# Kernel tuning notes

Hardware: AMD Instinct MI355X
Metric: run time of the kernel (lower is better)

The kernel has to match this reference:

```python
import jax, jax.numpy as jnp
import numpy as np

HOP = 768
NCB = 14
DIM = 512
VOCAB = 1024
W_SCALE = 0.02  # keep conv stacks numerically tame


def conv1d(x, w, b, stride=1, padding=0):
    # x: [B,C,L], w: [O,I,K] (torch layout), b: [O]
    y = jax.lax.conv_general_dilated(
        x, w, window_strides=(stride,), padding=[(padding, padding)],
        dimension_numbers=('NCH', 'OIH', 'NCH'))
    return y + b[None, :, None]


def conv_transpose1d(x, w, b, stride, padding):
    # torch ConvTranspose1d weight layout: (in, out, k)
    k = w.shape[2]
    w2 = jnp.flip(jnp.transpose(w, (1, 0, 2)), axis=2)  # -> OIH
    y = jax.lax.conv_general_dilated(
        x, w2, window_strides=(1,),
        padding=[(k - 1 - padding, k - 1 - padding)],
        lhs_dilation=(stride,),
        dimension_numbers=('NCH', 'OIH', 'NCH'))
    return y + b[None, :, None]


def setup_inputs() -> dict:
    key = jax.random.key(0)
    ks = jax.random.split(key, 16)
    f = lambda k, shp, s=W_SCALE: jax.random.normal(k, shp, dtype=jnp.float32) * s
    B, T = 2, 98304  # T = 768 * 128
    return {
        'audio': jax.random.normal(ks[0], (B, 1, T), dtype=jnp.float32),
        'codebooks': jax.random.normal(ks[1], (NCB, VOCAB, DIM), dtype=jnp.float32),
        'ew1': f(ks[2], (256, 1, 7)), 'eb1': f(ks[3], (256,)),
        'ew2': f(ks[4], (512, 256, 5)), 'eb2': f(ks[5], (512,)),
        'ew3': f(ks[6], (NCB * DIM, 512, 3)), 'eb3': f(ks[7], (NCB * DIM,)),
        'dw1': f(ks[8], (NCB * DIM, 512, 5)), 'db1': f(ks[9], (512,)),
        'dw2': f(ks[10], (256, 512, 5)), 'db2': f(ks[11], (256,)),
        'dw3': f(ks[12], (1, 256, 7)), 'db3': f(ks[13], (1,)),
    }


def reference(audio, codebooks, ew1, eb1, ew2, eb2, ew3, eb3,
              dw1, db1, dw2, db2, dw3, db3):
    B = audio.shape[0]
    # ---- encoder ----
    h = jax.nn.relu(conv1d(audio, ew1, eb1, stride=1, padding=3))
    h = jax.nn.relu(conv1d(h, ew2, eb2, stride=HOP, padding=2))
    h = conv1d(h, ew3, eb3, stride=1, padding=1)          # [B, NCB*DIM, S]
    S = h.shape[-1]
    emb = h.reshape(B, NCB, DIM, S).transpose(0, 1, 3, 2)  # [B, NCB, S, DIM]
    # ---- VQ: per-codebook squared L2 distance + argmin (same argmin as cdist) ----
    d2 = (jnp.sum(emb * emb, axis=-1, keepdims=True)            # [B,NCB,S,1]
          - 2.0 * jnp.einsum('bksd,kvd->bksv', emb, codebooks)  # [B,NCB,S,V]
          + jnp.sum(codebooks * codebooks, axis=-1)[None, :, None, :])
    codes = jnp.argmin(d2, axis=-1)                        # [B, NCB, S] int
    # ---- decode: embedding lookup + transposed conv decoder ----
    q = codebooks[jnp.arange(NCB)[None, :, None], codes]   # [B, NCB, S, DIM]
    q = q.transpose(0, 1, 3, 2).reshape(B, NCB * DIM, S)   # [B, NCB*DIM, S]
    a = jax.nn.relu(conv_transpose1d(q, dw1, db1, stride=HOP, padding=2))
    a = jax.nn.relu(conv1d(a, dw2, db2, stride=1, padding=2))
    a = jnp.tanh(conv1d(a, dw3, db3, stride=1, padding=3))
    return a  # [B, 1, (S-1)*HOP + 1]
```

## Files before the change

### kernel.cpp

```cpp
#include <hip/hip_runtime.h>
#include <hip/hip_bf16.h>
#include <math.h>

#define T_IN 98304
#define SS 128
#define NBATCH 2
#define NN 256
#define C1 256
#define C2 512
#define C3 7168
#define NCBK 14
#define DIMV 512
#define VOC 1024
#define TOUT 97537
#define HOP 768

#define OFF_CBN    0L
#define OFF_AB1    14336L
#define OFF_AB2    14848L
#define OFF_CCONST 15104L
#define OFF_H2C    15120L
#define OFF_H2XH   146192L
#define OFF_H2XL   342800L
#define OFF_H3H    539408L
#define OFF_H3L    1456912L
#define OFF_SCORES 2374416L
#define OFF_X1H    2374416L
#define OFF_X1L    2538256L
#define OFF_EW3PH  2374416L
#define OFF_EW3PL  5126928L
#define OFF_DW1T   539408L
#define OFF_XH     539408L
#define OFF_XL     3488528L
#define OFF_CODES  9714448L
#define OFF_QBF    9718032L
#define OFF_A1RAW  10635536L
#define OFF_A2ACT  11290896L

typedef __attribute__((ext_vector_type(8))) short short8;
typedef __attribute__((ext_vector_type(4))) float f32x4;

static __device__ inline ushort f2bf(float x) {
  __hip_bfloat16 h = __float2bfloat16(x);
  return *reinterpret_cast<ushort*>(&h);
}

static __device__ inline void split8(const float4 x0, const float4 x1,
                                     short8& h, short8& l) {
  float xs[8] = {x0.x, x0.y, x0.z, x0.w, x1.x, x1.y, x1.z, x1.w};
  #pragma unroll
  for (int e = 0; e < 8; ++e) {
    uint b = __float_as_uint(xs[e]);
    h[e] = (short)(b >> 16);
    float r = xs[e] - __uint_as_float(b & 0xffff0000u);
    l[e] = (short)(__float_as_uint(r) >> 16);
  }
}

__global__ void k_cbn(const float* __restrict__ cb, float* __restrict__ cbn) {
  int row = blockIdx.x * 4 + (threadIdx.x >> 6);
  int lane = threadIdx.x & 63;
  const float* p = cb + (long)row * DIMV;
  float s = 0.f;
  for (int d = lane; d < DIMV; d += 64) { float x = p[d]; s += x * x; }
  for (int off = 32; off; off >>= 1) s += __shfl_down(s, off);
  if (lane == 0) cbn[row] = s;
}

__global__ __launch_bounds__(256) void k_prep_ab2(const float* __restrict__ db1,
    const float* __restrict__ dw2, const float* __restrict__ db2,
    float* __restrict__ ab1, float* __restrict__ ab2) {
  __shared__ float red[256];
  int o = blockIdx.x, t = threadIdx.x;
  if (o == 0) { ab1[t] = fmaxf(db1[t], 0.f); ab1[t + 256] = fmaxf(db1[t + 256], 0.f); }
  const float* wp = dw2 + (long)o * C2 * 5;
  float acc = 0.f;
  #pragma unroll
  for (int h = 0; h < 2; ++h) {
    int c = t + h * 256;
    const float* p = wp + c * 5;
    float wsum = p[0] + p[1] + p[2] + p[3] + p[4];
    acc = fmaf(wsum, fmaxf(db1[c], 0.f), acc);
  }
  red[t] = acc;
  __syncthreads();
  for (int off = 128; off; off >>= 1) {
    if (t < off) red[t] += red[t + off];
    __syncthreads();
  }
  if (t == 0) ab2[o] = fmaxf(red[0] + db2[o], 0.f);
}

__global__ __launch_bounds__(256) void k_prep_c(const float* __restrict__ dw3,
    const float* __restrict__ db3, const float* __restrict__ ab2,
    float* __restrict__ cconst) {
  __shared__ float red[256];
  int t = threadIdx.x;
  float wsum3 = 0.f;
  #pragma unroll
  for (int j = 0; j < 7; ++j) wsum3 += dw3[t*7+j];
  red[t] = wsum3 * ab2[t];
  __syncthreads();
  for (int off = 128; off; off >>= 1) {
    if (t < off) red[t] += red[t + off];
    __syncthreads();
  }
  if (t == 0) cconst[0] = tanhf(red[0] + db3[0]);
}

__global__ __launch_bounds__(256) void k_enc1(const float* __restrict__ audio,
    const float* __restrict__ ew1, const float* __restrict__ eb1,
    ushort* __restrict__ X1h, ushort* __restrict__ X1l) {
  int n = blockIdx.x, ic = threadIdx.x;
  int b = n >> 7, s = n & 127;
  const float* ap = audio + (long)b * T_IN;
  int base = HOP * s - 5;
  float a[11];
  #pragma unroll
  for (int w = 0; w < 11; ++w) {
    int ai = base + w;
    a[w] = (ai >= 0 && ai < T_IN) ? ap[ai] : 0.f;
  }
  float w1[7];
  #pragma unroll
  for (int j = 0; j < 7; ++j) w1[j] = ew1[ic*7+j];
  float b1 = eb1[ic];
  long off = (long)n * 1280 + ic * 5;
  #pragma unroll
  for (int jj = 0; jj < 5; ++jj) {
    int tcol = HOP * s + jj - 2;
    float v = 0.f;
    if (tcol >= 0) {
      float acc = b1;
      #pragma unroll
      for (int j = 0; j < 7; ++j) acc = fmaf(w1[j], a[jj + j], acc);
      v = fmaxf(acc, 0.f);
    }
    uint bi = __float_as_uint(v);
    X1h[off + jj] = (ushort)(bi >> 16);
    float r = v - __uint_as_float(bi & 0xffff0000u);
    X1l[off + jj] = (ushort)(__float_as_uint(r) >> 16);
  }
}

__global__ __launch_bounds__(256) void gemm_enc2(const float* __restrict__ ew2,
    const ushort* __restrict__ X1h, const ushort* __restrict__ X1l,
    const float* __restrict__ eb2, float* __restrict__ h2c) {
  __shared__ __align__(16) float red[4 * 2048];
  const int tid = threadIdx.x;
  const int w = tid >> 6, lane = tid & 63;
  const int l15 = lane & 15, quad = lane >> 4;
  const int m0 = blockIdx.x * 32, n0 = blockIdx.y * 64;
  const int kbase = w * 320;
  f32x4 acc[2][4] = {};
  const float*  aB = ew2 + (long)(m0 + l15) * 1280 + kbase + quad * 8;
  const ushort* bhB = X1h + (long)(n0 + l15) * 1280 + kbase + quad * 8;
  const ushort* blB = X1l + (long)(n0 + l15) * 1280 + kbase + quad * 8;
  for (int k0 = 0; k0 < 320; k0 += 32) {
    short8 ah[2], al[2], bh[4], bl[4];
    #pragma unroll
    for (int f = 0; f < 2; ++f) {
      const float* ap = aB + (long)f * 16 * 1280 + k0;
      float4 x0 = *(const float4*)ap;
      float4 x1 = *(const float4*)(ap + 4);
      split8(x0, x1, ah[f], al[f]);
    }
    #pragma unroll
    for (int f = 0; f < 4; ++f) {
      bh[f] = *(const short8*)(bhB + (long)f * 16 * 1280 + k0);
      bl[f] = *(const short8*)(blB + (long)f * 16 * 1280 + k0);
    }
    #pragma unroll
    for (int i = 0; i < 2; ++i)
      #pragma unroll
      for (int j = 0; j < 4; ++j) {
        acc[i][j] = __builtin_amdgcn_mfma_f32_16x16x32_bf16(ah[i], bh[j], acc[i][j], 0, 0, 0);
        acc[i][j] = __builtin_amdgcn_mfma_f32_16x16x32_bf16(ah[i], bl[j], acc[i][j], 0, 0, 0);
        acc[i][j] = __builtin_amdgcn_mfma_f32_16x16x32_bf16(al[i], bh[j], acc[i][j], 0, 0, 0);
      }
  }
  #pragma unroll
  for (int i = 0; i < 2; ++i)
    #pragma unroll
    for (int j = 0; j < 4; ++j)
      *(float4*)&red[w * 2048 + (i * 4 + j) * 256 + lane * 4] = *(float4*)&acc[i][j];
  __syncthreads();
  #pragma unroll
  for (int q = 0; q < 2; ++q) {
    const int c = 2 * w + q;
    const int i = c >> 2, j = c & 3;
    float4 s = make_float4(0.f, 0.f, 0.f, 0.f);
    #pragma unroll
    for (int g = 0; g < 4; ++g) {
      float4 t4 = *(const float4*)&red[g * 2048 + c * 256 + lane * 4];
      s.x += t4.x; s.y += t4.y; s.z += t4.z; s.w += t4.w;
    }
    const int obase = m0 + i * 16 + quad * 4;
    float4 bias = *(const float4*)(eb2 + obase);
    const int n = n0 + j * 16 + l15;
    float4 out;
    out.x = fmaxf(s.x + bias.x, 0.f);
    out.y = fmaxf(s.y + bias.y, 0.f);
    out.z = fmaxf(s.z + bias.z, 0.f);
    out.w = fmaxf(s.w + bias.w, 0.f);
    *(float4*)(h2c + (long)n * C2 + obase) = out;
  }
}

__global__ void k_h2x(const float* __restrict__ h2c, ushort* __restrict__ h2xph,
                      ushort* __restrict__ h2xpl) {
  int idx = blockIdx.x * 256 + threadIdx.x;
  const int total = NN * 1536;
  for (; idx < total; idx += gridDim.x * 256) {
    int grp = idx >> 9;
    int r = idx & 511;
    int e = r & 7, lane = r >> 3;
    int quad = lane >> 4, l15 = lane & 15;
    int nt = grp / 48, kt = grp - nt * 48;
    int n = nt * 16 + l15;
    int k = kt * 32 + quad * 8 + e;
    int ic = k / 3, j = k - ic * 3;
    int s2 = (n & 127) + j - 1;
    int b = n >> 7;
    float v = (s2 >= 0 && s2 < SS) ? h2c[(long)(b*SS + s2)*C2 + ic] : 0.f;
    uint bi = __float_as_uint(v);
    h2xph[idx] = (ushort)(bi >> 16);
    float rr = v - __uint_as_float(bi & 0xffff0000u);
    h2xpl[idx] = (ushort)(__float_as_uint(rr) >> 16);
  }
}

__global__ __launch_bounds__(256) void k_ew3p(const float* __restrict__ ew3,
    ushort* __restrict__ ph, ushort* __restrict__ pl, int mrow0) {
  int o8 = blockIdx.x * 256 + threadIdx.x;
  const int total = 3584 * 1536 / 8;
  if (o8 >= total) return;
  int frag = o8 >> 6, lane = o8 & 63;
  int quad = lane >> 4, l15 = lane & 15;
  int mtL = frag / 48, kt = frag - mtL * 48;
  int m = mrow0 + mtL * 16 + l15;
  int k = kt * 32 + quad * 8;
  const float* s = ew3 + (long)m * 1536 + k;
  float4 x0 = *(const float4*)s;
  float4 x1 = *(const float4*)(s + 4);
  short8 h, l;
  split8(x0, x1, h, l);
  long off = (long)o8 * 8;
  *(short8*)(ph + off) = h;
  *(short8*)(pl + off) = l;
}

__global__ __launch_bounds__(256) void gemm_h3(const ushort* __restrict__ aH,
    const ushort* __restrict__ aL, const ushort* __restrict__ bH,
    const ushort* __restrict__ bL, const float* __restrict__ eb3,
    ushort* __restrict__ h3ph, ushort* __restrict__ h3pl, int mrow0) {
  __shared__ __align__(16) float red[4 * 4096];
  const int tid = threadIdx.x;
  const int w = tid >> 6, lane = tid & 63;
  const int l15 = lane & 15, quad = lane >> 4;
  const int bid = blockIdx.x;
  const int xcd = bid & 7, q = bid >> 3;
  const int mchunk = xcd * 7 + (q >> 2);
  const int nchunk = q & 3;
  const int mtL0 = mchunk * 4, nt0 = nchunk * 4, n0 = nchunk * 64;
  const int kt0 = w * 12;
  f32x4 acc[4][4] = {};
  const ushort* aHB = aH + ((long)(mtL0 * 48 + kt0)) * 512 + lane * 8;
  const ushort* aLB = aL + ((long)(mtL0 * 48 + kt0)) * 512 + lane * 8;
  const ushort* bHB = bH + ((long)(nt0 * 48 + kt0)) * 512 + lane * 8;
  const ushort* bLB = bL + ((long)(nt0 * 48 + kt0)) * 512 + lane * 8;
  for (int kt = 0; kt < 12; ++kt) {
    short8 ah[4], al[4], bh[4], bl[4];
    #pragma unroll
    for (int f = 0; f < 4; ++f) {
      long o = ((long)(f * 48 + kt)) * 512;
      ah[f] = *(const short8*)(aHB + o);
      al[f] = *(const short8*)(aLB + o);
      bh[f] = *(const short8*)(bHB + o);
      bl[f] = *(const short8*)(bLB + o);
    }
    #pragma unroll
    for (int i = 0; i < 4; ++i)
      #pragma unroll
      for (int j = 0; j < 4; ++j) {
        acc[i][j] = __builtin_amdgcn_mfma_f32_16x16x32_bf16(ah[i], bh[j], acc[i][j], 0, 0, 0);
        acc[i][j] = __builtin_amdgcn_mfma_f32_16x16x32_bf16(ah[i], bl[j], acc[i][j], 0, 0, 0);
        acc[i][j] = __builtin_amdgcn_mfma_f32_16x16x32_bf16(al[i], bh[j], acc[i][j], 0, 0, 0);
      }
  }
  #pragma unroll
  for (int i = 0; i < 4; ++i)
    #pragma unroll
    for (int j = 0; j < 4; ++j)
      *(float4*)&red[w * 4096 + (i * 4 + j) * 256 + lane * 4] = *(float4*)&acc[i][j];
  __syncthreads();
  const int mg0 = mrow0 + mchunk * 64 + w * 16 + quad * 4;
  float4 bias = *(const float4*)(eb3 + mg0);
  const int ktS = mg0 >> 5, quadk = (mg0 >> 3) & 3, es = mg0 & 7;
  #pragma unroll
  for (int j = 0; j < 4; ++j) {
    float4 s = *(const float4*)&red[(w * 4 + j) * 256 + lane * 4];
    #pragma unroll
    for (int r = 1; r < 4; ++r) {
      float4 tt = *(const float4*)&red[r * 4096 + (w * 4 + j) * 256 + lane * 4];
      s.x += tt.x; s.y += tt.y; s.z += tt.z; s.w += tt.w;
    }
    const int n = n0 + j * 16 + l15;
    float v0 = s.x + bias.x;
    float v1 = s.y + bias.y;
    float v2 = s.z + bias.z;
    float v3 = s.w + bias.w;
    uint b0 = __float_as_uint(v0), b1 = __float_as_uint(v1);
    uint b2 = __float_as_uint(v2), b3 = __float_as_uint(v3);
    uint2 hp;
    hp.x = (b0 >> 16) | (b1 & 0xffff0000u);
    hp.y = (b2 >> 16) | (b3 & 0xffff0000u);
    float r0 = v0 - __uint_as_float(b0 & 0xffff0000u);
    float r1 = v1 - __uint_as_float(b1 & 0xffff0000u);
    float r2 = v2 - __uint_as_float(b2 & 0xffff0000u);
    float r3 = v3 - __uint_as_float(b3 & 0xffff0000u);
    uint2 lp;
    lp.x = (__float_as_uint(r0) >> 16) | (__float_as_uint(r1) & 0xffff0000u);
    lp.y = (__float_as_uint(r2) >> 16) | (__float_as_uint(r3) & 0xffff0000u);
    long off = ((long)((n >> 4) * 224 + ktS)) * 512 + (quadk * 16 + (n & 15)) * 8 + es;
    *(uint2*)(h3ph + off) = hp;
    *(uint2*)(h3pl + off) = lp;
  }
}

__global__ __launch_bounds__(256) void gemm_scores(const float* __restrict__ cb,
    const ushort* __restrict__ h3ph, const ushort* __restrict__ h3pl,
    const float* __restrict__ cbn, float* __restrict__ scores) {
  __shared__ __align__(16) float red[4 * 4096];
  const int tid = threadIdx.x;
  const int w = tid >> 6, lane = tid & 63;
  const int l15 = lane & 15, quad = lane >> 4;
  const int m0 = blockIdx.x * 64, n0 = blockIdx.y * 64, z = blockIdx.z;
  const int kbase = w * 128;
  f32x4 acc[4][4] = {};
  const float*  aB = cb + (long)z * VOC * DIMV + (long)(m0 + l15) * 512 + kbase + quad * 8;
  const ushort* bHB = h3ph + ((long)((n0 >> 4) * 224 + z * 16 + (kbase >> 5))) * 512 + lane * 8;
  const ushort* bLB = h3pl + ((long)((n0 >> 4) * 224 + z * 16 + (kbase >> 5))) * 512 + lane * 8;
  for (int k0 = 0; k0 < 128; k0 += 32) {
    short8 ah[4], al[4], bh[4], bl[4];
    #pragma unroll
    for (int f = 0; f < 4; ++f) {
      const float* ap = aB + (long)f * 16 * 512 + k0;
      float4 x0 = *(const float4*)ap;
      float4 x1 = *(const float4*)(ap + 4);
      split8(x0, x1, ah[f], al[f]);
      long o = ((long)(f * 224) + (k0 >> 5)) * 512;
      bh[f] = *(const short8*)(bHB + o);
      bl[f] = *(const short8*)(bLB + o);
    }
    #pragma unroll
    for (int i = 0; i < 4; ++i)
      #pragma unroll
      for (int j = 0; j < 4; ++j) {
        acc[i][j] = __builtin_amdgcn_mfma_f32_16x16x32_bf16(ah[i], bh[j], acc[i][j], 0, 0, 0);
        acc[i][j] = __builtin_amdgcn_mfma_f32_16x16x32_bf16(ah[i], bl[j], acc[i][j], 0, 0, 0);
        acc[i][j] = __builtin_amdgcn_mfma_f32_16x16x32_bf16(al[i], bh[j], acc[i][j], 0, 0, 0);
      }
  }
  #pragma unroll
  for (int i = 0; i < 4; ++i)
    #pragma unroll
    for (int j = 0; j < 4; ++j)
      *(float4*)&red[w * 4096 + (i * 4 + j) * 256 + lane * 4] = *(float4*)&acc[i][j];
  __syncthreads();
  const int vbase = m0 + w * 16 + quad * 4;
  float4 cn = *(const float4*)(cbn + z * VOC + vbase);
  #pragma unroll
  for (int j = 0; j < 4; ++j) {
    float4 s = *(const float4*)&red[(w * 4 + j) * 256 + lane * 4];
    #pragma unroll
    for (int r = 1; r < 4; ++r) {
      float4 tt = *(const float4*)&red[r * 4096 + (w * 4 + j) * 256 + lane * 4];
      s.x += tt.x; s.y += tt.y; s.z += tt.z; s.w += tt.w;
    }
    const int n = n0 + j * 16 + l15;
    float4 out;
    out.x = cn.x - 2.f * s.x;
    out.y = cn.y - 2.f * s.y;
    out.z = cn.z - 2.f * s.z;
    out.w = cn.w - 2.f * s.w;
    *(float4*)(scores + ((long)z * NN + n) * VOC + vbase) = out;
  }
}

__global__ void k_argmin(const float* __restrict__ scores, int* __restrict__ codes) {
  int row = blockIdx.x;
  int lane = threadIdx.x;
  const float* p = scores + (long)row * VOC;
  float best = 3.4e38f; int bi = 0;
  for (int i = 0; i < 16; ++i) {
    int v = i * 64 + lane;
    float x = p[v];
    if (x < best) { best = x; bi = v; }
  }
  for (int off = 32; off; off >>= 1) {
    float ob = __shfl_down(best, off);
    int oi = __shfl_down(bi, off);
    if (ob < best || (ob == best && oi < bi)) { best = ob; bi = oi; }
  }
  if (lane == 0) codes[row] = bi;
}

__global__ __launch_bounds__(256) void k_dw1t(const float* __restrict__ dw1,
                                              ushort* __restrict__ dw1p) {
  __shared__ __align__(16) ushort T[64 * 72];
  int t = threadIdx.x;
  int k0 = blockIdx.x * 64, m0 = blockIdx.y * 64;
  int kk = t >> 2, mj = (t & 3) * 16;
  const float* src = dw1 + (long)(k0 + kk) * 2560 + m0 + mj;
  float x[16];
  *(float4*)&x[0]  = *(const float4*)(src);
  *(float4*)&x[4]  = *(const float4*)(src + 4);
  *(float4*)&x[8]  = *(const float4*)(src + 8);
  *(float4*)&x[12] = *(const float4*)(src + 12);
  #pragma unroll
  for (int l = 0; l < 16; ++l)
    T[(mj + l) * 72 + kk] = f2bf(x[l]);
  __syncthreads();
  int mo = t >> 2, kc = (t & 3) * 16;
  const int m = m0 + mo;
  const int mt = m >> 4, l15 = m & 15;
  #pragma unroll
  for (int h = 0; h < 2; ++h) {
    const int kk0 = kc + h * 8;
    const int kglob = k0 + kk0;
    const int kt = kglob >> 5;
    const int quad = (kglob >> 3) & 3;
    uint4 u = *(const uint4*)&T[mo * 72 + kk0];
    *(uint4*)(dw1p + ((long)(mt * 224 + kt)) * 512 + (quad * 16 + l15) * 8) = u;
  }
}

__global__ void k_gather_qbf(const float* __restrict__ cb, const int* __restrict__ codes,
                             ushort* __restrict__ qp) {
  int o = blockIdx.x * 256 + threadIdx.x;
  const int total = NN * C3 / 8;
  if (o >= total) return;
  int frag = o >> 6, r = o & 63;
  int quad = r >> 4, l15 = r & 15;
  int nt = frag / 224, kt = frag - nt * 224;
  int n = nt * 16 + l15;
  int kglob = kt * 32 + quad * 8;
  int kcb = kglob >> 9, d0 = kglob & 511;
  int code = codes[kcb * NN + n];
  const float* s = cb + ((long)(kcb * VOC + code)) * DIMV + d0;
  float4 x0 = *(const float4*)s;
  float4 x1 = *(const float4*)(s + 4);
  uint4 u;
  u.x = (uint)f2bf(x0.x) | ((uint)f2bf(x0.y) << 16);
  u.y = (uint)f2bf(x0.z) | ((uint)f2bf(x0.w) << 16);
  u.z = (uint)f2bf(x1.x) | ((uint)f2bf(x1.y) << 16);
  u.w = (uint)f2bf(x1.z) | ((uint)f2bf(x1.w) << 16);
  ((uint4*)qp)[o] = u;
}

__global__ __launch_bounds__(1024) void gemm_a1_mfma(const ushort* __restrict__ dw1p,
    const ushort* __restrict__ qp, float* __restrict__ a1raw) {
  __shared__ __align__(16) float red[4 * 4096];
  const int tid = threadIdx.x;
  const int w = tid >> 6, lane = tid & 63;
  const int l15 = lane & 15, quad = lane >> 4;
  const int mt0 = blockIdx.x * 4, nt0 = blockIdx.y * 4;
  const int kt0 = w * 14;
  f32x4 acc[4][4] = {};
  const ushort* aB = dw1p + ((long)(mt0 * 224 + kt0)) * 512 + lane * 8;
  const ushort* bB = qp   + ((long)(nt0 * 224 + kt0)) * 512 + lane * 8;
  #pragma unroll 2
  for (int kt = 0; kt < 14; ++kt) {
    short8 ah[4], bh[4];
    #pragma unroll
    for (int f = 0; f < 4; ++f) {
      ah[f] = *(const short8*)(aB + ((long)(f * 224 + kt)) * 512);
      bh[f] = *(const short8*)(bB + ((long)(f * 224 + kt)) * 512);
    }
    #pragma unroll
    for (int i = 0; i < 4; ++i)
      #pragma unroll
      for (int j = 0; j < 4; ++j)
        acc[i][j] = __builtin_amdgcn_mfma_f32_16x16x32_bf16(ah[i], bh[j], acc[i][j], 0, 0, 0);
  }
  float4 rsum = make_float4(0.f, 0.f, 0.f, 0.f);
  #pragma unroll
  for (int r = 0; r < 4; ++r) {
    if ((w >> 2) == r) {
      #pragma unroll
      for (int i = 0; i < 4; ++i)
        #pragma unroll
        for (int j = 0; j < 4; ++j)
          *(float4*)&red[(w & 3) * 4096 + (i * 4 + j) * 256 + lane * 4] = *(float4*)&acc[i][j];
    }
    __syncthreads();
    #pragma unroll
    for (int g = 0; g < 4; ++g) {
      float4 t4 = *(const float4*)&red[g * 4096 + w * 256 + lane * 4];
      rsum.x += t4.x; rsum.y += t4.y; rsum.z += t4.z; rsum.w += t4.w;
    }
    __syncthreads();
  }
  const int ci = w >> 2, cj = w & 3;
  const int n = nt0 * 16 + cj * 16 + l15;
  const int mb = mt0 * 16 + ci * 16 + quad * 4;
  float v[4] = {rsum.x, rsum.y, rsum.z, rsum.w};
  #pragma unroll
  for (int reg = 0; reg < 4; ++reg) {
    int m = mb + reg;
    int c = m / 5, jj = m - c * 5;
    a1raw[((long)(n * 5 + jj)) * C2 + c] = v[reg];
  }
}

__global__ void k_x2(const float* __restrict__ a1raw, const float* __restrict__ ab1g,
                     const float* __restrict__ db1, ushort* __restrict__ Xh,
                     ushort* __restrict__ Xl) {
  int idx = blockIdx.x * 256 + threadIdx.x;
  const int total = 2304 * 2560;
  for (; idx < total; idx += gridDim.x * 256) {
    int nu = idx / 2560, ck = idx - nu * 2560;
    int n = nu / 9, u = nu - n * 9;
    int c = ck / 5, jj = ck - c * 5;
    int w = u + jj;
    int s = n & 127;
    int tc = HOP * s - 6 + w;
    float v;
    if (tc < 0 || tc > TOUT - 1) v = 0.f;
    else if (w >= 4 && w <= 8)
      v = fmaxf(db1[c] + a1raw[((long)(n * 5 + (w - 4))) * C2 + c], 0.f);
    else v = ab1g[c];
    uint bi = __float_as_uint(v);
    Xh[idx] = (ushort)(bi >> 16);
    float rr = v - __uint_as_float(bi & 0xffff0000u);
    Xl[idx] = (ushort)(__float_as_uint(rr) >> 16);
  }
}

__global__ __launch_bounds__(256) void gemm_dec2(const float* __restrict__ dw2,
    const ushort* __restrict__ Xh, const ushort* __restrict__ Xl,
    const float* __restrict__ db2, float* __restrict__ a2act) {
  __shared__ __align__(16) float red[4 * 4096];
  const int tid = threadIdx.x;
  const int w = tid >> 6, lane = tid & 63;
  const int l15 = lane & 15, quad = lane >> 4;
  const int m0 = blockIdx.x * 64, n0 = blockIdx.y * 64;
  const int kbase = w * 640;
  f32x4 acc[4][4] = {};
  const float*  aB = dw2 + (long)(m0 + l15) * 2560 + kbase + quad * 8;
  const ushort* bhB = Xh + (long)(n0 + l15) * 2560 + kbase + quad * 8;
  const ushort* blB = Xl + (long)(n0 + l15) * 2560 + kbase + quad * 8;
  for (int k0 = 0; k0 < 640; k0 += 32) {
    short8 ah[4], al[4], bh[4], bl[4];
    #pragma unroll
    for (int f = 0; f < 4; ++f) {
      const float* ap = aB + (long)f * 16 * 2560 + k0;
      float4 x0 = *(const float4*)ap;
      float4 x1 = *(const float4*)(ap + 4);
      split8(x0, x1, ah[f], al[f]);
      bh[f] = *(const short8*)(bhB + (long)f * 16 * 2560 + k0);
      bl[f] = *(const short8*)(blB + (long)f * 16 * 2560 + k0);
    }
    #pragma unroll
    for (int i = 0; i < 4; ++i)
      #pragma unroll
      for (int j = 0; j < 4; ++j) {
        acc[i][j] = __builtin_amdgcn_mfma_f32_16x16x32_bf16(ah[i], bh[j], acc[i][j], 0, 0, 0);
        acc[i][j] = __builtin_amdgcn_mfma_f32_16x16x32_bf16(ah[i], bl[j], acc[i][j], 0, 0, 0);
        acc[i][j] = __builtin_amdgcn_mfma_f32_16x16x32_bf16(al[i], bh[j], acc[i][j], 0, 0, 0);
      }
  }
  #pragma unroll
  for (int i = 0; i < 4; ++i)
    #pragma unroll
    for (int j = 0; j < 4; ++j)
      *(float4*)&red[w * 4096 + (i * 4 + j) * 256 + lane * 4] = *(float4*)&acc[i][j];
  __syncthreads();
  const int mb = m0 + w * 16 + quad * 4;
  float4 bias = *(const float4*)(db2 + mb);
  #pragma unroll
  for (int j = 0; j < 4; ++j) {
    float4 s = *(const float4*)&red[(w * 4 + j) * 256 + lane * 4];
    #pragma unroll
    for (int r = 1; r < 4; ++r) {
      float4 tt = *(const float4*)&red[r * 4096 + (w * 4 + j) * 256 + lane * 4];
      s.x += tt.x; s.y += tt.y; s.z += tt.z; s.w += tt.w;
    }
    const int nu = n0 + j * 16 + l15;
    float4 out;
    out.x = fmaxf(s.x + bias.x, 0.f);
    out.y = fmaxf(s.y + bias.y, 0.f);
    out.z = fmaxf(s.z + bias.z, 0.f);
    out.w = fmaxf(s.w + bias.w, 0.f);
    *(float4*)(a2act + (long)nu * C1 + mb) = out;
  }
}

__global__ void k_fill(float* __restrict__ outp, const float* __restrict__ cconst) {
  float v = cconst[0];
  int idx = blockIdx.x * 256 + threadIdx.x;
  const int total = NBATCH * TOUT;
  for (; idx < total; idx += gridDim.x * 256) outp[idx] = v;
}

__global__ __launch_bounds__(256) void k_dec3(const float* __restrict__ a2act,
    const float* __restrict__ ab2g, const float* __restrict__ dw3,
    const float* __restrict__ db3, float* __restrict__ outp) {
  __shared__ float sa2[9 * C1];
  __shared__ float sb[C1];
  int n = blockIdx.x;
  int s = n & 127, b = n >> 7;
  int t = threadIdx.x;
  for (int i = t; i < 9 * C1; i += 256) sa2[i] = a2act[(long)n * 9 * C1 + i];
  sb[t] = ab2g[t];
  __syncthreads();
  int wv = t >> 6, lane = t & 63;
  float b3 = db3[0];
  for (int w15 = wv; w15 < 15; w15 += 4) {
    int tc = HOP * s - 7 + w15;
    if (tc < 0 || tc > TOUT - 1) continue;
    float part = 0.f;
    for (int cc = lane; cc < C1; cc += 64) {
      #pragma unroll
      for (int j = 0; j < 7; ++j) {
        int wcol = tc + j - 3;
        float x;
        if (wcol < 0 || wcol > TOUT - 1) x = 0.f;
        else {
          int du = wcol - (HOP * s - 4);
          x = (du >= 0 && du <= 8) ? sa2[du * C1 + cc] : sb[cc];
        }
        part = fmaf(dw3[cc*7+j], x, part);
      }
    }
    for (int off = 32; off; off >>= 1) part += __shfl_down(part, off);
    if (lane == 0) outp[(long)b * TOUT + tc] = tanhf(part + b3);
  }
}

extern "C" void kernel_launch(void* const* d_in, const int* in_sizes, int n_in,
                              void* d_out, int out_size, void* d_ws, size_t ws_size,
                              hipStream_t stream) {
  const float* audio = (const float*)d_in[0];
  const float* cb    = (const float*)d_in[1];
  const float* ew1   = (const float*)d_in[2];
  const float* eb1   = (const float*)d_in[3];
  const float* ew2   = (const float*)d_in[4];
  const float* eb2   = (const float*)d_in[5];
  const float* ew3   = (const float*)d_in[6];
  const float* eb3   = (const float*)d_in[7];
  const float* dw1   = (const float*)d_in[8];
  const float* db1   = (const float*)d_in[9];
  const float* dw2   = (const float*)d_in[10];
  const float* db2   = (const float*)d_in[11];
  const float* dw3   = (const float*)d_in[12];
  const float* db3   = (const float*)d_in[13];
  float* outp = (float*)d_out;
  float* ws = (float*)d_ws;

  float*  cbn    = ws + OFF_CBN;
  float*  ab1    = ws + OFF_AB1;
  float*  ab2    = ws + OFF_AB2;
  float*  cconst = ws + OFF_CCONST;
  float*  h2c    = ws + OFF_H2C;
  ushort* h2xph  = (ushort*)(ws + OFF_H2XH);
  ushort* h2xpl  = (ushort*)(ws + OFF_H2XL);
  ushort* h3ph   = (ushort*)(ws + OFF_H3H);
  ushort* h3pl   = (ushort*)(ws + OFF_H3L);
  float*  scores = ws + OFF_SCORES;
  ushort* X1h    = (ushort*)(ws + OFF_X1H);
  ushort* X1l    = (ushort*)(ws + OFF_X1L);
  ushort* ew3ph  = (ushort*)(ws + OFF_EW3PH);
  ushort* ew3pl  = (ushort*)(ws + OFF_EW3PL);
  ushort* dw1p   = (ushort*)(ws + OFF_DW1T);
  ushort* Xh     = (ushort*)(ws + OFF_XH);
  ushort* Xl     = (ushort*)(ws + OFF_XL);
  int*    codes  = (int*)(ws + OFF_CODES);
  ushort* qp     = (ushort*)(ws + OFF_QBF);
  float*  a1raw  = ws + OFF_A1RAW;
  float*  a2act  = ws + OFF_A2ACT;

  k_cbn<<<3584, 256, 0, stream>>>(cb, cbn);
  k_prep_ab2<<<C1, 256, 0, stream>>>(db1, dw2, db2, ab1, ab2);
  k_prep_c<<<1, 256, 0, stream>>>(dw3, db3, ab2, cconst);
  k_enc1<<<NN, 256, 0, stream>>>(audio, ew1, eb1, X1h, X1l);
  gemm_enc2<<<dim3(16, 4), 256, 0, stream>>>(ew2, X1h, X1l, eb2, h2c);
  k_h2x<<<384, 256, 0, stream>>>(h2c, h2xph, h2xpl);
  k_ew3p<<<2688, 256, 0, stream>>>(ew3, ew3ph, ew3pl, 0);
  gemm_h3<<<224, 256, 0, stream>>>(ew3ph, ew3pl, h2xph, h2xpl, eb3, h3ph, h3pl, 0);
  k_ew3p<<<2688, 256, 0, stream>>>(ew3, ew3ph, ew3pl, 3584);
  gemm_h3<<<224, 256, 0, stream>>>(ew3ph, ew3pl, h2xph, h2xpl, eb3, h3ph, h3pl, 3584);
  gemm_scores<<<dim3(16, 4, 14), 256, 0, stream>>>(cb, h3ph, h3pl, cbn, scores);
  k_argmin<<<NCBK * NN, 64, 0, stream>>>(scores, codes);
  k_dw1t<<<dim3(112, 40), 256, 0, stream>>>(dw1, dw1p);
  k_gather_qbf<<<896, 256, 0, stream>>>(cb, codes, qp);
  gemm_a1_mfma<<<dim3(40, 4), 1024, 0, stream>>>(dw1p, qp, a1raw);
  k_x2<<<4096, 256, 0, stream>>>(a1raw, ab1, db1, Xh, Xl);
  gemm_dec2<<<dim3(4, 36), 256, 0, stream>>>(dw2, Xh, Xl, db2, a2act);
  k_fill<<<256, 256, 0, stream>>>(outp, cconst);
  k_dec3<<<NN, 256, 0, stream>>>(a2act, ab2, dw3, db3, outp);
}
```

Measured before the change: 419.5 us.

## Pre-split dw2 and store dec2 operands in MFMA fragment-packed layout

Adds a kernel that splits dw2 into bf16 hi/lo halves once, stored in a fragment-tiled layout. k_x2 now writes the X activations in the same 16x32 fragment order. gemm_dec2 then loads contiguous 16-byte fragments per lane instead of doing strided row loads and converting fp32 weights inside the loop. This costs an extra launch and extra weight traffic, and it reuses the a1raw workspace region, which is safe only because k_x2 has already consumed a1raw.

```diff
diff --git a/kernel.cpp b/kernel.cpp
--- a/kernel.cpp
+++ b/kernel.cpp
@@ -35,6 +35,8 @@
 #define OFF_CODES  9714448L
 #define OFF_QBF    9718032L
 #define OFF_A1RAW  10635536L
+#define OFF_DW2PH  10635536L
+#define OFF_DW2PL  10963216L
 #define OFF_A2ACT  11290896L
 
 typedef __attribute__((ext_vector_type(8))) short short8;
@@ -520,7 +522,13 @@
   int idx = blockIdx.x * 256 + threadIdx.x;
   const int total = 2304 * 2560;
   for (; idx < total; idx += gridDim.x * 256) {
-    int nu = idx / 2560, ck = idx - nu * 2560;
+    int grp = idx >> 9;
+    int r = idx & 511;
+    int e = r & 7, lane = r >> 3;
+    int quad = lane >> 4, l15 = lane & 15;
+    int nt = grp / 80, kt = grp - nt * 80;
+    int nu = nt * 16 + l15;
+    int ck = kt * 32 + quad * 8 + e;
     int n = nu / 9, u = nu - n * 9;
     int c = ck / 5, jj = ck - c * 5;
     int w = u + jj;
@@ -538,29 +546,51 @@
   }
 }
 
-__global__ __launch_bounds__(256) void gemm_dec2(const float* __restrict__ dw2,
-    const ushort* __restrict__ Xh, const ushort* __restrict__ Xl,
-    const float* __restrict__ db2, float* __restrict__ a2act) {
+__global__ __launch_bounds__(256) void k_dw2p(const float* __restrict__ dw2,
+    ushort* __restrict__ ph, ushort* __restrict__ pl) {
+  int o8 = blockIdx.x * 256 + threadIdx.x;
+  const int total = 256 * 2560 / 8;
+  if (o8 >= total) return;
+  int frag = o8 >> 6, lane = o8 & 63;
+  int quad = lane >> 4, l15 = lane & 15;
+  int mt = frag / 80, kt = frag - mt * 80;
+  int m = mt * 16 + l15;
+  int k = kt * 32 + quad * 8;
+  const float* s = dw2 + (long)m * 2560 + k;
+  float4 x0 = *(const float4*)s;
+  float4 x1 = *(const float4*)(s + 4);
+  short8 h, l;
+  split8(x0, x1, h, l);
+  long off = (long)o8 * 8;
+  *(short8*)(ph + off) = h;
+  *(short8*)(pl + off) = l;
+}
+
+__global__ __launch_bounds__(256) void gemm_dec2(const ushort* __restrict__ aH,
+    const ushort* __restrict__ aL, const ushort* __restrict__ bH,
+    const ushort* __restrict__ bL, const float* __restrict__ db2,
+    float* __restrict__ a2act) {
   __shared__ __align__(16) float red[4 * 4096];
   const int tid = threadIdx.x;
   const int w = tid >> 6, lane = tid & 63;
   const int l15 = lane & 15, quad = lane >> 4;
-  const int m0 = blockIdx.x * 64, n0 = blockIdx.y * 64;
-  const int kbase = w * 640;
+  const int mt0 = blockIdx.x * 4, nt0 = blockIdx.y * 4;
+  const int m0 = mt0 * 16, n0 = nt0 * 16;
+  const int kt0 = w * 20;
   f32x4 acc[4][4] = {};
-  const float*  aB = dw2 + (long)(m0 + l15) * 2560 + kbase + quad * 8;
-  const ushort* bhB = Xh + (long)(n0 + l15) * 2560 + kbase + quad * 8;
-  const ushort* blB = Xl + (long)(n0 + l15) * 2560 + kbase + quad * 8;
-  for (int k0 = 0; k0 < 640; k0 += 32) {
+  const ushort* aHB = aH + ((long)(mt0 * 80 + kt0)) * 512 + lane * 8;
+  const ushort* aLB = aL + ((long)(mt0 * 80 + kt0)) * 512 + lane * 8;
+  const ushort* bHB = bH + ((long)(nt0 * 80 + kt0)) * 512 + lane * 8;
+  const ushort* bLB = bL + ((long)(nt0 * 80 + kt0)) * 512 + lane * 8;
+  for (int kt = 0; kt < 20; ++kt) {
     short8 ah[4], al[4], bh[4], bl[4];
     #pragma unroll
     for (int f = 0; f < 4; ++f) {
-      const float* ap = aB + (long)f * 16 * 2560 + k0;
-      float4 x0 = *(const float4*)ap;
-      float4 x1 = *(const float4*)(ap + 4);
-      split8(x0, x1, ah[f], al[f]);
-      bh[f] = *(const short8*)(bhB + (long)f * 16 * 2560 + k0);
-      bl[f] = *(const short8*)(blB + (long)f * 16 * 2560 + k0);
+      long o = ((long)(f * 80 + kt)) * 512;
+      ah[f] = *(const short8*)(aHB + o);
+      al[f] = *(const short8*)(aLB + o);
+      bh[f] = *(const short8*)(bHB + o);
+      bl[f] = *(const short8*)(bLB + o);
     }
     #pragma unroll
     for (int i = 0; i < 4; ++i)
@@ -679,6 +709,8 @@
   int*    codes  = (int*)(ws + OFF_CODES);
   ushort* qp     = (ushort*)(ws + OFF_QBF);
   float*  a1raw  = ws + OFF_A1RAW;
+  ushort* dw2ph  = (ushort*)(ws + OFF_DW2PH);
+  ushort* dw2pl  = (ushort*)(ws + OFF_DW2PL);
   float*  a2act  = ws + OFF_A2ACT;
 
   k_cbn<<<3584, 256, 0, stream>>>(cb, cbn);
@@ -697,7 +729,8 @@
   k_gather_qbf<<<896, 256, 0, stream>>>(cb, codes, qp);
   gemm_a1_mfma<<<dim3(40, 4), 1024, 0, stream>>>(dw1p, qp, a1raw);
   k_x2<<<4096, 256, 0, stream>>>(a1raw, ab1, db1, Xh, Xl);
-  gemm_dec2<<<dim3(4, 36), 256, 0, stream>>>(dw2, Xh, Xl, db2, a2act);
+  k_dw2p<<<320, 256, 0, stream>>>(dw2, dw2ph, dw2pl);
+  gemm_dec2<<<dim3(4, 36), 256, 0, stream>>>(dw2ph, dw2pl, Xh, Xl, db2, a2act);
   k_fill<<<256, 256, 0, stream>>>(outp, cconst);
   k_dec3<<<NN, 256, 0, stream>>>(a2act, ab2, dw3, db3, outp);
 }
```

Result: no change. 419.0 us (-0.1%).
